# Performance work log

Measured on AMD Instinct MI355X. Metric: run time of the kernel, lower is better.

Reference implementation:

```python
import jax, jax.numpy as jnp
import numpy as np

V, C, H, L, T, B = 256, 1024, 16, 6, 1024, 8
HS = C // H
EPS = 1e-5


def setup_inputs() -> dict:
    key = jax.random.key(0)
    ks = jax.random.split(key, 20)
    s = 0.02
    inp = {
        "idx": jax.random.randint(ks[0], (B, T), 0, V),
        "tok_emb": jax.random.normal(ks[1], (V, C), jnp.float32) * s,
        "pos_emb": jax.random.normal(ks[2], (T, C), jnp.float32) * s,
        "Wq": jax.random.normal(ks[3], (L, C, C), jnp.float32) * s,
        "Wk": jax.random.normal(ks[4], (L, C, C), jnp.float32) * s,
        "Wv": jax.random.normal(ks[5], (L, C, C), jnp.float32) * s,
        "Wo": jax.random.normal(ks[6], (L, C, C), jnp.float32) * s,
        "bo": jnp.zeros((L, C), jnp.float32),
        "ln1_g": jnp.ones((L, C), jnp.float32),
        "ln1_b": jnp.zeros((L, C), jnp.float32),
        "ln2_g": jnp.ones((L, C), jnp.float32),
        "ln2_b": jnp.zeros((L, C), jnp.float32),
        "W1": jax.random.normal(ks[7], (L, C, 4 * C), jnp.float32) * s,
        "b1": jnp.zeros((L, 4 * C), jnp.float32),
        "W2": jax.random.normal(ks[8], (L, 4 * C, C), jnp.float32) * s,
        "b2": jnp.zeros((L, C), jnp.float32),
        "lnf_g": jnp.ones((C,), jnp.float32),
        "lnf_b": jnp.zeros((C,), jnp.float32),
        "Whead": jax.random.normal(ks[9], (C, V), jnp.float32) * s,
        "bhead": jnp.zeros((V,), jnp.float32),
    }
    return inp


def _ln(x, g, b):
    mu = jnp.mean(x, axis=-1, keepdims=True)
    var = jnp.mean(jnp.square(x - mu), axis=-1, keepdims=True)
    return (x - mu) * jax.lax.rsqrt(var + EPS) * g + b


def reference(idx, tok_emb, pos_emb, Wq, Wk, Wv, Wo, bo, ln1_g, ln1_b,
              ln2_g, ln2_b, W1, b1, W2, b2, lnf_g, lnf_b, Whead, bhead):
    Bv, Tv = idx.shape
    x = tok_emb[idx] + pos_emb[:Tv]  # [B,T,C]
    causal = jnp.tril(jnp.ones((Tv, Tv), bool))  # [T,T]
    scale = 1.0 / np.sqrt(HS)
    neg_inf = jnp.finfo(x.dtype).min
    for l in range(L):
        h = _ln(x, ln1_g[l], ln1_b[l])
        q = (h @ Wq[l]).reshape(Bv, Tv, H, HS)
        k = (h @ Wk[l]).reshape(Bv, Tv, H, HS)
        v = (h @ Wv[l]).reshape(Bv, Tv, H, HS)
        wei = jnp.einsum("bthd,bshd->bhts", q, k) * scale  # [B,H,T,T]
        wei = jnp.where(causal, wei, neg_inf)
        wei = jax.nn.softmax(wei, axis=-1)
        att = jnp.einsum("bhts,bshd->bthd", wei, v).reshape(Bv, Tv, C)
        x = x + att @ Wo[l] + bo[l]
        h2 = _ln(x, ln2_g[l], ln2_b[l])
        x = x + jax.nn.relu(h2 @ W1[l] + b1[l]) @ W2[l] + b2[l]
    x = _ln(x, lnf_g, lnf_b)
    logits = x @ Whead + bhead  # [B,T,V]
    return logits
```

## Files before the change

### kernel.cpp

```cpp
#include <hip/hip_runtime.h>

typedef unsigned short u16;
typedef unsigned int   u32;
typedef __attribute__((ext_vector_type(4))) float  f32x4;
typedef __attribute__((ext_vector_type(8))) __bf16 bf16x8;
typedef __attribute__((ext_vector_type(8))) short  s16x8;
typedef __attribute__((ext_vector_type(4))) unsigned short u16x4;

#define DEVFN __device__ __forceinline__

DEVFN float bf2f(u16 u) {
    u32 v = ((u32)u) << 16;
    return __builtin_bit_cast(float, v);
}
DEVFN u16 f2bf(float f) {
    u32 u = __builtin_bit_cast(u32, f);
    u32 r = u + 0x7FFFu + ((u >> 16) & 1u);
    return (u16)(r >> 16);
}

DEVFN void gload16(const void* g, void* l) {
    __builtin_amdgcn_global_load_lds(
        (const __attribute__((address_space(1))) void*)g,
        (__attribute__((address_space(3))) void*)l, 16, 0, 0);
}

__global__ __launch_bounds__(256) void embed_k(const int* __restrict__ idx,
                                               const float* __restrict__ tok,
                                               const float* __restrict__ pos,
                                               float* __restrict__ x)
{
    int i   = blockIdx.x * 256 + threadIdx.x;
    int row = i >> 8;
    int c   = (i & 255) << 2;
    int t   = row & 1023;
    int tk  = idx[row];
    float4 a = *(const float4*)&tok[(size_t)tk * 1024 + c];
    float4 p = *(const float4*)&pos[(size_t)t * 1024 + c];
    float4 r; r.x = a.x + p.x; r.y = a.y + p.y; r.z = a.z + p.z; r.w = a.w + p.w;
    *(float4*)&x[(size_t)row * 1024 + c] = r;
}

__global__ __launch_bounds__(256) void transpose_k(const float* __restrict__ W,
                                                   u16* __restrict__ Wt, int K, int N)
{
    __shared__ float tile[32][33];
    int n0 = blockIdx.x * 32, k0 = blockIdx.y * 32;
    int xx = threadIdx.x, ty = threadIdx.y;
#pragma unroll
    for (int yy = 0; yy < 4; ++yy) {
        int y = ty + yy * 8;
        tile[y][xx] = W[(size_t)(k0 + y) * N + n0 + xx];
    }
    __syncthreads();
#pragma unroll
    for (int yy = 0; yy < 4; ++yy) {
        int y = ty + yy * 8;
        Wt[(size_t)(n0 + y) * K + k0 + xx] = f2bf(tile[xx][y]);
    }
}

__global__ __launch_bounds__(256) void ln_k(const float* __restrict__ x,
                                            const float* __restrict__ g,
                                            const float* __restrict__ b,
                                            u16* __restrict__ out)
{
    const int row = blockIdx.x, tid = threadIdx.x;
    const float4 v = *(const float4*)&x[(size_t)row * 1024 + tid * 4];
    __shared__ float red[8];
    float s = v.x + v.y + v.z + v.w;
#pragma unroll
    for (int off = 32; off > 0; off >>= 1) s += __shfl_down(s, off);
    const int lane = tid & 63, wv = tid >> 6;
    if (lane == 0) red[wv] = s;
    __syncthreads();
    const float mu = (red[0] + red[1] + red[2] + red[3]) * (1.0f / 1024.0f);
    const float dx = v.x - mu, dy = v.y - mu, dz = v.z - mu, dw = v.w - mu;
    float s2 = dx * dx + dy * dy + dz * dz + dw * dw;
#pragma unroll
    for (int off = 32; off > 0; off >>= 1) s2 += __shfl_down(s2, off);
    if (lane == 0) red[4 + wv] = s2;
    __syncthreads();
    const float var = (red[4] + red[5] + red[6] + red[7]) * (1.0f / 1024.0f);
    const float rs  = rsqrtf(var + 1e-5f);
    const float4 gv = *(const float4*)&g[tid * 4];
    const float4 bv = *(const float4*)&b[tid * 4];
    u16x4 o;
    o.x = f2bf(dx * rs * gv.x + bv.x);
    o.y = f2bf(dy * rs * gv.y + bv.y);
    o.z = f2bf(dz * rs * gv.z + bv.z);
    o.w = f2bf(dw * rs * gv.w + bv.w);
    *(u16x4*)&out[(size_t)row * 1024 + tid * 4] = o;
}

template <int MODE>
__global__ __launch_bounds__(256) void gemm_bt(const u16* __restrict__ A,
                                               const u16* __restrict__ Bt,
                                               const float* __restrict__ bias,
                                               float* __restrict__ RES,
                                               u16* __restrict__ Ob,
                                               float* __restrict__ Of,
                                               int N, int K, int ntx)
{
    __shared__ __align__(16) u16 As[2][128 * 32];
    __shared__ __align__(16) u16 Bs[2][128 * 32];
    const int tid  = threadIdx.x;
    const int lane = tid & 63, wave = tid >> 6;
    const int wr = wave >> 1, wc = wave & 1;
    const int l15 = lane & 15, l4 = lane >> 4;

    const int nwg = (int)gridDim.x;
    const int bid = (int)blockIdx.x;
    const int swz = (bid & 7) * (nwg >> 3) + (bid >> 3);
    const int n0 = (swz % ntx) * 128, m0 = (swz / ntx) * 128;

    f32x4 acc[4][4];
    const f32x4 zz = {0.f, 0.f, 0.f, 0.f};
#pragma unroll
    for (int i = 0; i < 4; ++i)
#pragma unroll
        for (int j = 0; j < 4; ++j) acc[i][j] = zz;

    const int r0 = tid >> 2, q0q = (tid & 3) * 8;
    const int r1 = (tid + 256) >> 2, q1q = ((tid + 256) & 3) * 8;
    const u16* Arow0 = &A [(size_t)(m0 + r0) * K + q0q];
    const u16* Brow0 = &Bt[(size_t)(n0 + r0) * K + q0q];
    const u16* Arow1 = &A [(size_t)(m0 + r1) * K + q1q];
    const u16* Brow1 = &Bt[(size_t)(n0 + r1) * K + q1q];

    gload16(Arow0, &As[0][tid * 8]);
    gload16(Brow0, &Bs[0][tid * 8]);
    gload16(Arow1, &As[0][(tid + 256) * 8]);
    gload16(Brow1, &Bs[0][(tid + 256) * 8]);
    __syncthreads();

    const int S = K >> 5;
    int cur = 0;
    for (int s = 0; s < S; ++s) {
        if (s + 1 < S) {
            const int kn = (s + 1) << 5;
            gload16(Arow0 + kn, &As[cur ^ 1][tid * 8]);
            gload16(Brow0 + kn, &Bs[cur ^ 1][tid * 8]);
            gload16(Arow1 + kn, &As[cur ^ 1][(tid + 256) * 8]);
            gload16(Brow1 + kn, &Bs[cur ^ 1][(tid + 256) * 8]);
        }
        s16x8 af[4], bw[4];
#pragma unroll
        for (int i = 0; i < 4; ++i)
            af[i] = *(const s16x8*)&As[cur][(wr * 64 + i * 16 + l15) * 32 + l4 * 8];
#pragma unroll
        for (int j = 0; j < 4; ++j)
            bw[j] = *(const s16x8*)&Bs[cur][(wc * 64 + j * 16 + l15) * 32 + l4 * 8];
#pragma unroll
        for (int i = 0; i < 4; ++i)
#pragma unroll
            for (int j = 0; j < 4; ++j)
                acc[i][j] = __builtin_amdgcn_mfma_f32_16x16x32_bf16(
                    __builtin_bit_cast(bf16x8, af[i]),
                    __builtin_bit_cast(bf16x8, bw[j]), acc[i][j], 0, 0, 0);
        __syncthreads();
        cur ^= 1;
    }

#pragma unroll
    for (int i = 0; i < 4; ++i) {
        const int rb = m0 + wr * 64 + i * 16 + l4 * 4;
#pragma unroll
        for (int j = 0; j < 4; ++j) {
            const int col = n0 + wc * 64 + j * 16 + l15;
            const float bval = (MODE == 0) ? 0.0f : bias[col];
#pragma unroll
            for (int r = 0; r < 4; ++r) {
                const size_t o = (size_t)(rb + r) * N + col;
                const float v = acc[i][j][r];
                if (MODE == 0)      Ob[o] = f2bf(v);
                else if (MODE == 1) RES[o] += v + bval;
                else if (MODE == 2) Ob[o] = f2bf(fmaxf(v + bval, 0.0f));
                else                Of[o] = v + bval;
            }
        }
    }
}

__global__ __launch_bounds__(256) void attn_mfma_k(const u16* __restrict__ QKV,
                                                   u16* __restrict__ Og)
{
    const int qt  = (int)(gridDim.x - 1 - blockIdx.x);
    const int bh  = blockIdx.y;
    const int b   = bh >> 4, h = bh & 15;
    const int tid = threadIdx.x;
    const int wq  = tid >> 6, lane = tid & 63;
    const int l15 = lane & 15, l4 = lane >> 4;

    __shared__ __align__(16) u16 Ks[2][64][72];
    __shared__ __align__(16) u16 Vt[2][64][72];
    __shared__ __align__(16) u16 Ps[4][16][68];

    const int qrow0 = qt * 128 + wq * 32;

    const u16* Qbase = QKV + (size_t)b * 1024 * 3072 + h * 64;
    const u16* Kbase = Qbase + 1024;
    const u16* Vbase = Qbase + 2048;

    s16x8 aQ[2][2];
#pragma unroll
    for (int qi = 0; qi < 2; ++qi) {
        const u16* qsrc = Qbase + (size_t)(qrow0 + qi * 16 + l15) * 3072;
        aQ[qi][0] = *(const s16x8*)(qsrc + l4 * 8);
        aQ[qi][1] = *(const s16x8*)(qsrc + 32 + l4 * 8);
    }

    f32x4 O[2][4];
    const f32x4 zz = {0.f, 0.f, 0.f, 0.f};
    float mrow[2][4], lrow[2][4];
#pragma unroll
    for (int qi = 0; qi < 2; ++qi) {
#pragma unroll
        for (int dj = 0; dj < 4; ++dj) O[qi][dj] = zz;
#pragma unroll
        for (int r = 0; r < 4; ++r) { mrow[qi][r] = -3.0e38f; lrow[qi][r] = 0.f; }
    }

    const int srow = tid >> 3;
    const int soff = (tid & 7) * 8;
    const int vp   = tid >> 3;
    const int vdg  = tid & 7;
    const int vc   = (vp + 4 * vdg) & 31;

    const int ntiles = 2 * qt + 2;
    s16x8 kr0, kr1, vr0, vr1;

    {
        const u16* kb0 = Kbase + (size_t)srow * 3072 + soff;
        kr0 = *(const s16x8*)kb0;
        kr1 = *(const s16x8*)(kb0 + (size_t)32 * 3072);
        const u16* vb0 = Vbase + (size_t)(2 * vp) * 3072 + vdg * 8;
        vr0 = *(const s16x8*)vb0;
        vr1 = *(const s16x8*)(vb0 + 3072);
        *(s16x8*)&Ks[0][srow][soff]      = kr0;
        *(s16x8*)&Ks[0][srow + 32][soff] = kr1;
        u32* VtW = (u32*)&Vt[0][0][0];
#pragma unroll
        for (int e = 0; e < 8; ++e) {
            u32 pk = (u32)(u16)vr0[e] | ((u32)(u16)vr1[e] << 16);
            VtW[(vdg * 8 + e) * 36 + vc] = pk;
        }
    }
    __syncthreads();

    int cur = 0;
    for (int t = 0; t < ntiles; ++t) {
        const int kv0 = t * 64;
        const bool more = (t + 1 < ntiles);
        if (more) {
            const u16* kb0 = Kbase + (size_t)(kv0 + 64 + srow) * 3072 + soff;
            kr0 = *(const s16x8*)kb0;
            kr1 = *(const s16x8*)(kb0 + (size_t)32 * 3072);
            const u16* vb0 = Vbase + (size_t)(kv0 + 64 + 2 * vp) * 3072 + vdg * 8;
            vr0 = *(const s16x8*)vb0;
            vr1 = *(const s16x8*)(vb0 + 3072);
        }
        const u32* VtW = (const u32*)&Vt[cur][0][0];

#pragma unroll
        for (int qi = 0; qi < 2; ++qi) {
            const int qlo = qrow0 + qi * 16;
            if (kv0 > qlo + 15) continue;
            f32x4 S[4];
            __builtin_amdgcn_s_setprio(1);
#pragma unroll
            for (int kc = 0; kc < 4; ++kc) {
                f32x4 s = zz;
                s16x8 bK0 = *(const s16x8*)&Ks[cur][kc * 16 + l15][l4 * 8];
                s16x8 bK1 = *(const s16x8*)&Ks[cur][kc * 16 + l15][32 + l4 * 8];
                s = __builtin_amdgcn_mfma_f32_16x16x32_bf16(
                    __builtin_bit_cast(bf16x8, aQ[qi][0]), __builtin_bit_cast(bf16x8, bK0), s, 0, 0, 0);
                s = __builtin_amdgcn_mfma_f32_16x16x32_bf16(
                    __builtin_bit_cast(bf16x8, aQ[qi][1]), __builtin_bit_cast(bf16x8, bK1), s, 0, 0, 0);
#pragma unroll
                for (int r = 0; r < 4; ++r) S[kc][r] = s[r] * 0.125f;
            }
            __builtin_amdgcn_s_setprio(0);
            if (kv0 + 63 > qlo) {
#pragma unroll
                for (int kc = 0; kc < 4; ++kc) {
                    const int k = kv0 + kc * 16 + l15;
#pragma unroll
                    for (int r = 0; r < 4; ++r)
                        if (k > qlo + l4 * 4 + r) S[kc][r] = -3.0e38f;
                }
            }
            float mloc[4];
#pragma unroll
            for (int r = 0; r < 4; ++r)
                mloc[r] = fmaxf(fmaxf(S[0][r], S[1][r]), fmaxf(S[2][r], S[3][r]));
#pragma unroll
            for (int off = 1; off < 16; off <<= 1)
#pragma unroll
                for (int r = 0; r < 4; ++r) mloc[r] = fmaxf(mloc[r], __shfl_xor(mloc[r], off));
            float alpha[4];
#pragma unroll
            for (int r = 0; r < 4; ++r) {
                const float mnew = fmaxf(mrow[qi][r], mloc[r]);
                alpha[r] = __expf(mrow[qi][r] - mnew);
                mrow[qi][r] = mnew;
            }
            float psum[4] = {0.f, 0.f, 0.f, 0.f};
#pragma unroll
            for (int kc = 0; kc < 4; ++kc)
#pragma unroll
                for (int r = 0; r < 4; ++r) {
                    const float p = __expf(S[kc][r] - mrow[qi][r]);
                    Ps[wq][l4 * 4 + r][kc * 16 + l15] = f2bf(p);
                    psum[r] += p;
                }
#pragma unroll
            for (int off = 1; off < 16; off <<= 1)
#pragma unroll
                for (int r = 0; r < 4; ++r) psum[r] += __shfl_xor(psum[r], off);
#pragma unroll
            for (int r = 0; r < 4; ++r) lrow[qi][r] = lrow[qi][r] * alpha[r] + psum[r];
#pragma unroll
            for (int dj = 0; dj < 4; ++dj)
#pragma unroll
                for (int r = 0; r < 4; ++r) O[qi][dj][r] *= alpha[r];
            __builtin_amdgcn_s_setprio(1);
#pragma unroll
            for (int kk = 0; kk < 2; ++kk) {
                s16x8 aP = *(const s16x8*)&Ps[wq][l15][kk * 32 + l4 * 8];
#pragma unroll
                for (int dj = 0; dj < 4; ++dj) {
                    const int d = dj * 16 + l15;
                    const int c = (kk * 16 + l4 * 4 + 4 * ((d >> 3) & 7)) & 31;
                    s16x8 bV = *(const s16x8*)&VtW[d * 36 + c];
                    O[qi][dj] = __builtin_amdgcn_mfma_f32_16x16x32_bf16(
                        __builtin_bit_cast(bf16x8, aP), __builtin_bit_cast(bf16x8, bV),
                        O[qi][dj], 0, 0, 0);
                }
            }
            __builtin_amdgcn_s_setprio(0);
        }

        if (more) {
            *(s16x8*)&Ks[cur ^ 1][srow][soff]      = kr0;
            *(s16x8*)&Ks[cur ^ 1][srow + 32][soff] = kr1;
            u32* VtWn = (u32*)&Vt[cur ^ 1][0][0];
#pragma unroll
            for (int e = 0; e < 8; ++e) {
                u32 pk = (u32)(u16)vr0[e] | ((u32)(u16)vr1[e] << 16);
                VtWn[(vdg * 8 + e) * 36 + vc] = pk;
            }
        }
        __syncthreads();
        cur ^= 1;
    }
#pragma unroll
    for (int qi = 0; qi < 2; ++qi)
#pragma unroll
        for (int dj = 0; dj < 4; ++dj)
#pragma unroll
            for (int r = 0; r < 4; ++r) {
                const size_t o = ((size_t)(b * 1024 + qrow0 + qi * 16 + l4 * 4 + r)) * 1024
                               + h * 64 + dj * 16 + l15;
                Og[o] = f2bf(O[qi][dj][r] / lrow[qi][r]);
            }
}

extern "C" void kernel_launch(void* const* d_in, const int* in_sizes, int n_in,
                              void* d_out, int out_size, void* d_ws, size_t ws_size,
                              hipStream_t stream)
{
    (void)in_sizes; (void)n_in; (void)out_size; (void)ws_size;
    const int*   idx  = (const int*)  d_in[0];
    const float* tok  = (const float*)d_in[1];
    const float* pos  = (const float*)d_in[2];
    const float* Wq   = (const float*)d_in[3];
    const float* Wk   = (const float*)d_in[4];
    const float* Wv   = (const float*)d_in[5];
    const float* Wo   = (const float*)d_in[6];
    const float* bo   = (const float*)d_in[7];
    const float* ln1g = (const float*)d_in[8];
    const float* ln1b = (const float*)d_in[9];
    const float* ln2g = (const float*)d_in[10];
    const float* ln2b = (const float*)d_in[11];
    const float* W1   = (const float*)d_in[12];
    const float* b1   = (const float*)d_in[13];
    const float* W2   = (const float*)d_in[14];
    const float* b2   = (const float*)d_in[15];
    const float* lnfg = (const float*)d_in[16];
    const float* lnfb = (const float*)d_in[17];
    const float* Wh   = (const float*)d_in[18];
    const float* bh   = (const float*)d_in[19];

    char* p = (char*)d_ws;
    float* x  = (float*)p; p += (size_t)8192 * 1024 * 4;
    u16* h    = (u16*)p;   p += (size_t)8192 * 1024 * 2;
    u16* qkv  = (u16*)p;   p += (size_t)8192 * 3072 * 2;
    u16* ab   = (u16*)p;   p += (size_t)8192 * 1024 * 2;
    u16* fb   = (u16*)p;   p += (size_t)8192 * 4096 * 2;
    u16* wqT  = (u16*)p;   p += (size_t)1024 * 1024 * 2;
    u16* wkT  = (u16*)p;   p += (size_t)1024 * 1024 * 2;
    u16* wvT  = (u16*)p;   p += (size_t)1024 * 1024 * 2;
    u16* woT  = (u16*)p;   p += (size_t)1024 * 1024 * 2;
    u16* w1T  = (u16*)p;   p += (size_t)1024 * 4096 * 2;
    u16* w2T  = (u16*)p;   p += (size_t)4096 * 1024 * 2;
    u16* whT  = (u16*)p;   p += (size_t)1024 * 256 * 2;

    const dim3 tb(32, 8);
    embed_k<<<8192, 256, 0, stream>>>(idx, tok, pos, x);
    for (int l = 0; l < 6; ++l) {
        transpose_k<<<dim3(32, 32),  tb, 0, stream>>>(Wq + (size_t)l * 1048576, wqT, 1024, 1024);
        transpose_k<<<dim3(32, 32),  tb, 0, stream>>>(Wk + (size_t)l * 1048576, wkT, 1024, 1024);
        transpose_k<<<dim3(32, 32),  tb, 0, stream>>>(Wv + (size_t)l * 1048576, wvT, 1024, 1024);
        transpose_k<<<dim3(32, 32),  tb, 0, stream>>>(Wo + (size_t)l * 1048576, woT, 1024, 1024);
        transpose_k<<<dim3(128, 32), tb, 0, stream>>>(W1 + (size_t)l * 4194304, w1T, 1024, 4096);
        transpose_k<<<dim3(32, 128), tb, 0, stream>>>(W2 + (size_t)l * 4194304, w2T, 4096, 1024);

        ln_k<<<8192, 256, 0, stream>>>(x, ln1g + l * 1024, ln1b + l * 1024, h);
        gemm_bt<0><<<1536, 256, 0, stream>>>(h, wqT, nullptr, nullptr, qkv, nullptr, 3072, 1024, 24);
        attn_mfma_k<<<dim3(8, 128), 256, 0, stream>>>(qkv, ab);
        gemm_bt<1><<<512,  256, 0, stream>>>(ab, woT, bo + l * 1024, x, nullptr, nullptr, 1024, 1024, 8);
        ln_k<<<8192, 256, 0, stream>>>(x, ln2g + l * 1024, ln2b + l * 1024, h);
        gemm_bt<2><<<2048, 256, 0, stream>>>(h, w1T, b1 + l * 4096, nullptr, fb, nullptr, 4096, 1024, 32);
        gemm_bt<1><<<512,  256, 0, stream>>>(fb, w2T, b2 + l * 1024, x, nullptr, nullptr, 1024, 4096, 8);
    }
    transpose_k<<<dim3(8, 32), tb, 0, stream>>>(Wh, whT, 1024, 256);
    ln_k<<<8192, 256, 0, stream>>>(x, lnfg, lnfb, h);
    gemm_bt<3><<<128, 256, 0, stream>>>(h, whT, bh, nullptr, nullptr, (float*)d_out, 256, 1024, 2);
}
```

Measured before the change: 2.777 ms.

## Merge per-layer weight transposes into one launch and single-buffer attention K/V

Replaces the six per-layer transpose launches with one kernel that picks its source matrix from the block index, which cuts launch overhead and tail effects. Separately, the attention kernel drops its double-buffered K/V shared-memory staging with register prefetch in favour of a single buffer loaded synchronously at the start of each tile, using two barriers per tile. That halves the attention kernel's LDS footprint and register pressure, which may raise occupancy, but global-load latency is no longer hidden behind compute.

Result: faster. 2.706 ms (-2.5%).

```diff
diff --git a/kernel.cpp b/kernel.cpp
--- a/kernel.cpp
+++ b/kernel.cpp
@@ -56,6 +56,46 @@
 #pragma unroll
     for (int yy = 0; yy < 4; ++yy) {
         int y = ty + yy * 8;
+        Wt[(size_t)(n0 + y) * K + k0 + xx] = f2bf(tile[xx][y]);
+    }
+}
+
+__global__ __launch_bounds__(256) void transpose_all_k(
+    const float* __restrict__ Wq, const float* __restrict__ Wk,
+    const float* __restrict__ Wv, const float* __restrict__ Wo,
+    const float* __restrict__ W1, const float* __restrict__ W2,
+    u16* __restrict__ qkvT, u16* __restrict__ woT,
+    u16* __restrict__ w1T, u16* __restrict__ w2T)
+{
+    __shared__ float tile[32][33];
+    const int id = blockIdx.x;
+    const float* W; u16* Wt; int K, N, bx, by;
+    if (id < 3072) {
+        const int m = id >> 10, t2 = id & 1023;
+        W = (m == 0) ? Wq : (m == 1) ? Wk : Wv;
+        Wt = qkvT + (size_t)m * 1024 * 1024;
+        K = 1024; N = 1024; bx = t2 & 31; by = t2 >> 5;
+    } else if (id < 4096) {
+        const int t2 = id - 3072;
+        W = Wo; Wt = woT; K = 1024; N = 1024; bx = t2 & 31; by = t2 >> 5;
+    } else if (id < 8192) {
+        const int t2 = id - 4096;
+        W = W1; Wt = w1T; K = 1024; N = 4096; bx = t2 & 127; by = t2 >> 7;
+    } else {
+        const int t2 = id - 8192;
+        W = W2; Wt = w2T; K = 4096; N = 1024; bx = t2 & 31; by = t2 >> 5;
+    }
+    const int n0 = bx * 32, k0 = by * 32;
+    const int xx = threadIdx.x, ty = threadIdx.y;
+#pragma unroll
+    for (int yy = 0; yy < 4; ++yy) {
+        const int y = ty + yy * 8;
+        tile[y][xx] = W[(size_t)(k0 + y) * N + n0 + xx];
+    }
+    __syncthreads();
+#pragma unroll
+    for (int yy = 0; yy < 4; ++yy) {
+        const int y = ty + yy * 8;
         Wt[(size_t)(n0 + y) * K + k0 + xx] = f2bf(tile[xx][y]);
     }
 }
@@ -192,9 +232,10 @@
     const int wq  = tid >> 6, lane = tid & 63;
     const int l15 = lane & 15, l4 = lane >> 4;
 
-    __shared__ __align__(16) u16 Ks[2][64][72];
-    __shared__ __align__(16) u16 Vt[2][64][72];
+    __shared__ __align__(16) u16 Ks[64][72];
+    __shared__ __align__(16) u16 Vt[64][72];
     __shared__ __align__(16) u16 Ps[4][16][68];
+    u32* VtW = (u32*)&Vt[0][0];
 
     const int qrow0 = qt * 128 + wq * 32;
 
@@ -225,42 +266,29 @@
     const int soff = (tid & 7) * 8;
     const int vp   = tid >> 3;
     const int vdg  = tid & 7;
-    const int vc   = (vp + 4 * vdg) & 31;
 
     const int ntiles = 2 * qt + 2;
-    s16x8 kr0, kr1, vr0, vr1;
-
-    {
-        const u16* kb0 = Kbase + (size_t)srow * 3072 + soff;
-        kr0 = *(const s16x8*)kb0;
-        kr1 = *(const s16x8*)(kb0 + (size_t)32 * 3072);
-        const u16* vb0 = Vbase + (size_t)(2 * vp) * 3072 + vdg * 8;
-        vr0 = *(const s16x8*)vb0;
-        vr1 = *(const s16x8*)(vb0 + 3072);
-        *(s16x8*)&Ks[0][srow][soff]      = kr0;
-        *(s16x8*)&Ks[0][srow + 32][soff] = kr1;
-        u32* VtW = (u32*)&Vt[0][0][0];
-#pragma unroll
-        for (int e = 0; e < 8; ++e) {
-            u32 pk = (u32)(u16)vr0[e] | ((u32)(u16)vr1[e] << 16);
-            VtW[(vdg * 8 + e) * 36 + vc] = pk;
-        }
-    }
-    __syncthreads();
-
-    int cur = 0;
     for (int t = 0; t < ntiles; ++t) {
         const int kv0 = t * 64;
-        const bool more = (t + 1 < ntiles);
-        if (more) {
-            const u16* kb0 = Kbase + (size_t)(kv0 + 64 + srow) * 3072 + soff;
-            kr0 = *(const s16x8*)kb0;
-            kr1 = *(const s16x8*)(kb0 + (size_t)32 * 3072);
-            const u16* vb0 = Vbase + (size_t)(kv0 + 64 + 2 * vp) * 3072 + vdg * 8;
-            vr0 = *(const s16x8*)vb0;
-            vr1 = *(const s16x8*)(vb0 + 3072);
+        __syncthreads();
+        {
+            const u16* kb0 = Kbase + (size_t)(kv0 + srow) * 3072 + soff;
+            *(s16x8*)&Ks[srow][soff]      = *(const s16x8*)kb0;
+            *(s16x8*)&Ks[srow + 32][soff] = *(const s16x8*)(kb0 + (size_t)32 * 3072);
         }
-        const u32* VtW = (const u32*)&Vt[cur][0][0];
+        {
+            const u16* vb0 = Vbase + (size_t)(kv0 + 2 * vp) * 3072 + vdg * 8;
+            s16x8 v0 = *(const s16x8*)vb0;
+            s16x8 v1 = *(const s16x8*)(vb0 + 3072);
+#pragma unroll
+            for (int e = 0; e < 8; ++e) {
+                const int d = vdg * 8 + e;
+                const int c = (vp + 4 * vdg) & 31;
+                u32 pk = (u32)(u16)v0[e] | ((u32)(u16)v1[e] << 16);
+                VtW[d * 36 + c] = pk;
+            }
+        }
+        __syncthreads();
 
 #pragma unroll
         for (int qi = 0; qi < 2; ++qi) {
@@ -271,8 +299,8 @@
 #pragma unroll
             for (int kc = 0; kc < 4; ++kc) {
                 f32x4 s = zz;
-                s16x8 bK0 = *(const s16x8*)&Ks[cur][kc * 16 + l15][l4 * 8];
-                s16x8 bK1 = *(const s16x8*)&Ks[cur][kc * 16 + l15][32 + l4 * 8];
+                s16x8 bK0 = *(const s16x8*)&Ks[kc * 16 + l15][l4 * 8];
+                s16x8 bK1 = *(const s16x8*)&Ks[kc * 16 + l15][32 + l4 * 8];
                 s = __builtin_amdgcn_mfma_f32_16x16x32_bf16(
                     __builtin_bit_cast(bf16x8, aQ[qi][0]), __builtin_bit_cast(bf16x8, bK0), s, 0, 0, 0);
                 s = __builtin_amdgcn_mfma_f32_16x16x32_bf16(
@@ -340,19 +368,6 @@
             }
             __builtin_amdgcn_s_setprio(0);
         }
-
-        if (more) {
-            *(s16x8*)&Ks[cur ^ 1][srow][soff]      = kr0;
-            *(s16x8*)&Ks[cur ^ 1][srow + 32][soff] = kr1;
-            u32* VtWn = (u32*)&Vt[cur ^ 1][0][0];
-#pragma unroll
-            for (int e = 0; e < 8; ++e) {
-                u32 pk = (u32)(u16)vr0[e] | ((u32)(u16)vr1[e] << 16);
-                VtWn[(vdg * 8 + e) * 36 + vc] = pk;
-            }
-        }
-        __syncthreads();
-        cur ^= 1;
     }
 #pragma unroll
     for (int qi = 0; qi < 2; ++qi)
@@ -405,16 +420,16 @@
     u16* w1T  = (u16*)p;   p += (size_t)1024 * 4096 * 2;
     u16* w2T  = (u16*)p;   p += (size_t)4096 * 1024 * 2;
     u16* whT  = (u16*)p;   p += (size_t)1024 * 256 * 2;
+    (void)wkT; (void)wvT;
 
     const dim3 tb(32, 8);
     embed_k<<<8192, 256, 0, stream>>>(idx, tok, pos, x);
     for (int l = 0; l < 6; ++l) {
-        transpose_k<<<dim3(32, 32),  tb, 0, stream>>>(Wq + (size_t)l * 1048576, wqT, 1024, 1024);
-        transpose_k<<<dim3(32, 32),  tb, 0, stream>>>(Wk + (size_t)l * 1048576, wkT, 1024, 1024);
-        transpose_k<<<dim3(32, 32),  tb, 0, stream>>>(Wv + (size_t)l * 1048576, wvT, 1024, 1024);
-        transpose_k<<<dim3(32, 32),  tb, 0, stream>>>(Wo + (size_t)l * 1048576, woT, 1024, 1024);
-        transpose_k<<<dim3(128, 32), tb, 0, stream>>>(W1 + (size_t)l * 4194304, w1T, 1024, 4096);
-        transpose_k<<<dim3(32, 128), tb, 0, stream>>>(W2 + (size_t)l * 4194304, w2T, 4096, 1024);
+        transpose_all_k<<<12288, tb, 0, stream>>>(
+            Wq + (size_t)l * 1048576, Wk + (size_t)l * 1048576,
+            Wv + (size_t)l * 1048576, Wo + (size_t)l * 1048576,
+            W1 + (size_t)l * 4194304, W2 + (size_t)l * 4194304,
+            wqT, woT, w1T, w2T);
 
         ln_k<<<8192, 256, 0, stream>>>(x, ln1g + l * 1024, ln1b + l * 1024, h);
         gemm_bt<0><<<1536, 256, 0, stream>>>(h, wqT, nullptr, nullptr, qkv, nullptr, 3072, 1024, 24);
```
